# Kernel optimization log

Measured on AMD Instinct MI355X. Metric: run time of the kernel, lower is better.

## Reference

```python
import jax, jax.numpy as jnp
import numpy as np

B, S, D, H = 2, 2048, 1024, 16
HD = D // H
EPS = 1e-5

def _ln(x, g, b):
    mu = jnp.mean(x, axis=-1, keepdims=True)
    var = jnp.var(x, axis=-1, keepdims=True)
    return (x - mu) * jax.lax.rsqrt(var + EPS) * g + b

def setup_inputs() -> dict:
    key = jax.random.key(0)
    ks = jax.random.split(key, 6)
    sc = lambda n: 1.0 / np.sqrt(n)
    return {
        "x": jax.random.normal(ks[0], (B, S, D), jnp.float32),
        "W_qkv": jax.random.normal(ks[1], (D, 3 * D), jnp.float32) * sc(D),
        "b_qkv": jnp.zeros((3 * D,), jnp.float32),
        "W_o": jax.random.normal(ks[2], (D, D), jnp.float32) * sc(D),
        "b_o": jnp.zeros((D,), jnp.float32),
        "W_fc": jax.random.normal(ks[3], (D, 4 * D), jnp.float32) * sc(D),
        "b_fc": jnp.zeros((4 * D,), jnp.float32),
        "W_pr": jax.random.normal(ks[4], (4 * D, D), jnp.float32) * sc(4 * D),
        "b_pr": jnp.zeros((D,), jnp.float32),
        "g1": jnp.ones((D,), jnp.float32),
        "beta1": jnp.zeros((D,), jnp.float32),
        "g2": jnp.ones((D,), jnp.float32),
        "beta2": jnp.zeros((D,), jnp.float32),
    }

def reference(x, W_qkv, b_qkv, W_o, b_o, W_fc, b_fc, W_pr, b_pr, g1, beta1, g2, beta2):
    # pre-norm attention
    h = _ln(x, g1, beta1)
    qkv = h @ W_qkv + b_qkv                      # [B,S,3D]
    q, k, v = jnp.split(qkv, 3, axis=-1)
    q = q.reshape(B, S, H, HD).transpose(0, 2, 1, 3)  # [B,H,S,hd]
    k = k.reshape(B, S, H, HD).transpose(0, 2, 1, 3)
    v = v.reshape(B, S, H, HD).transpose(0, 2, 1, 3)
    scores = jnp.einsum('bhqd,bhkd->bhqk', q, k) / np.sqrt(HD)
    causal = jnp.tril(jnp.ones((S, S), bool))
    scores = jnp.where(causal, scores, -jnp.inf)
    attn = jax.nn.softmax(scores, axis=-1)
    out = jnp.einsum('bhqk,bhkd->bhqd', attn, v)
    out = out.transpose(0, 2, 1, 3).reshape(B, S, D)
    x = x + out @ W_o + b_o
    # pre-norm MLP (exact erf GELU, matching torch F.gelu default)
    h2 = _ln(x, g2, beta2)
    h2 = jax.nn.gelu(h2 @ W_fc + b_fc, approximate=False)
    x = x + h2 @ W_pr + b_pr
    return x
```

## Files before the change

### kernel.cpp

```cpp
#include <hip/hip_runtime.h>
#include <cstdint>
#include <cstddef>

#define Bb 2
#define Ss 2048
#define Dd 1024
#define Hh 16

typedef __attribute__((ext_vector_type(8))) short short8;
typedef __attribute__((ext_vector_type(4))) short short4v;
typedef __attribute__((ext_vector_type(4))) float float4v;

__device__ inline short f2bf(float f) {
  unsigned u = __builtin_bit_cast(unsigned, f);
  u = (u + 0x7fffu + ((u >> 16) & 1u)) >> 16;
  return (short)u;
}

__device__ inline float bf2f(short s) {
  unsigned u = ((unsigned)(unsigned short)s) << 16;
  return __builtin_bit_cast(float, u);
}

__device__ inline void gl_lds16(const void* g, void* l) {
  __builtin_amdgcn_global_load_lds(
      (__attribute__((address_space(1))) void*)(void*)(g),
      (__attribute__((address_space(3))) void*)(l), 16, 0, 0);
}

#define MFMA(a, b, c) __builtin_amdgcn_mfma_f32_16x16x32_bf16((a), (b), (c), 0, 0, 0)

__device__ __forceinline__ void ln_row(const float* __restrict__ x,
                                       const float* __restrict__ g,
                                       const float* __restrict__ be,
                                       short* __restrict__ out, int row,
                                       float* red) {
  int tid = threadIdx.x;
  const float4* xr = (const float4*)(x + (size_t)row * Dd);
  float4 v = xr[tid];
  float s = v.x + v.y + v.z + v.w;
  float q = v.x * v.x + v.y * v.y + v.z * v.z + v.w * v.w;
#pragma unroll
  for (int off = 1; off < 64; off <<= 1) {
    s += __shfl_xor(s, off);
    q += __shfl_xor(q, off);
  }
  int w = tid >> 6;
  if ((tid & 63) == 0) { red[w] = s; red[4 + w] = q; }
  __syncthreads();
  s = red[0] + red[1] + red[2] + red[3];
  q = red[4] + red[5] + red[6] + red[7];
  float mu = s * (1.0f / Dd);
  float var = q * (1.0f / Dd) - mu * mu;
  float rstd = rsqrtf(var + 1e-5f);
  float4 gv = ((const float4*)g)[tid], bv = ((const float4*)be)[tid];
  short4v o;
  o.x = f2bf((v.x - mu) * rstd * gv.x + bv.x);
  o.y = f2bf((v.y - mu) * rstd * gv.y + bv.y);
  o.z = f2bf((v.z - mu) * rstd * gv.z + bv.z);
  o.w = f2bf((v.w - mu) * rstd * gv.w + bv.w);
  *(short4v*)(out + (size_t)row * Dd + tid * 4) = o;
}

__global__ __launch_bounds__(256) void prep_kernel(
    const float* __restrict__ W0, short* __restrict__ T0,
    const float* __restrict__ W1, short* __restrict__ T1,
    const float* __restrict__ W2, short* __restrict__ T2,
    const float* __restrict__ W3, short* __restrict__ T3,
    const float* __restrict__ x, const float* __restrict__ g1,
    const float* __restrict__ be1, short* __restrict__ h1) {
  __shared__ __align__(16) float t[32][33];
  int id = blockIdx.x;
  if (id >= 12288) {
    ln_row(x, g1, be1, h1, id - 12288, &t[0][0]);
    return;
  }
  const float* W; short* Wt; int N, K, tix;
  if (id < 3072)      { W = W0; Wt = T0; N = 3072; K = 1024; tix = id; }
  else if (id < 4096) { W = W1; Wt = T1; N = 1024; K = 1024; tix = id - 3072; }
  else if (id < 8192) { W = W2; Wt = T2; N = 4096; K = 1024; tix = id - 4096; }
  else                { W = W3; Wt = T3; N = 1024; K = 4096; tix = id - 8192; }
  int nx = N / 32;
  int n0 = (tix % nx) * 32, k0 = (tix / nx) * 32;
  int tx = threadIdx.x & 31, ty = threadIdx.x >> 5;
#pragma unroll
  for (int i = 0; i < 4; i++)
    t[ty + 8 * i][tx] = W[(size_t)(k0 + ty + 8 * i) * N + n0 + tx];
  __syncthreads();
#pragma unroll
  for (int i = 0; i < 4; i++)
    Wt[(size_t)(n0 + ty + 8 * i) * K + k0 + tx] = f2bf(t[tx][ty + 8 * i]);
}

__global__ __launch_bounds__(256) void reduce_ln_kernel(const float* __restrict__ x,
                                                        const float* __restrict__ bias,
                                                        const short* __restrict__ parts,
                                                        const float* __restrict__ g,
                                                        const float* __restrict__ be,
                                                        float* __restrict__ x1,
                                                        short* __restrict__ h2) {
  int row = blockIdx.x, tid = threadIdx.x;
  size_t base = (size_t)row * Dd + tid * 4;
  float4 v = *(const float4*)(x + base);
  float4 bv = ((const float4*)bias)[tid];
  v.x += bv.x; v.y += bv.y; v.z += bv.z; v.w += bv.w;
#pragma unroll
  for (int s = 0; s < 2; s++) {
    short4v p = *(const short4v*)(parts + (size_t)s * 4096 * Dd + base);
    v.x += bf2f(p.x); v.y += bf2f(p.y); v.z += bf2f(p.z); v.w += bf2f(p.w);
  }
  *(float4*)(x1 + base) = v;
  float s = v.x + v.y + v.z + v.w;
  float q = v.x * v.x + v.y * v.y + v.z * v.z + v.w * v.w;
#pragma unroll
  for (int off = 1; off < 64; off <<= 1) {
    s += __shfl_xor(s, off);
    q += __shfl_xor(q, off);
  }
  __shared__ float as_[4], aq_[4];
  int w = tid >> 6;
  if ((tid & 63) == 0) { as_[w] = s; aq_[w] = q; }
  __syncthreads();
  s = as_[0] + as_[1] + as_[2] + as_[3];
  q = aq_[0] + aq_[1] + aq_[2] + aq_[3];
  float mu = s * (1.0f / Dd);
  float var = q * (1.0f / Dd) - mu * mu;
  float rstd = rsqrtf(var + 1e-5f);
  float4 gv = ((const float4*)g)[tid], b2 = ((const float4*)be)[tid];
  short4v o;
  o.x = f2bf((v.x - mu) * rstd * gv.x + b2.x);
  o.y = f2bf((v.y - mu) * rstd * gv.y + b2.y);
  o.z = f2bf((v.z - mu) * rstd * gv.z + b2.z);
  o.w = f2bf((v.w - mu) * rstd * gv.w + b2.w);
  *(short4v*)(h2 + base) = o;
}

__global__ __launch_bounds__(256) void reduce_kernel(const float* __restrict__ src,
                                                     const float* __restrict__ bias,
                                                     const short* __restrict__ parts,
                                                     float* __restrict__ dst) {
  int row = blockIdx.x, tid = threadIdx.x;
  size_t base = (size_t)row * Dd + tid * 4;
  float4 v = *(const float4*)(src + base);
  float4 bv = ((const float4*)bias)[tid];
  v.x += bv.x; v.y += bv.y; v.z += bv.z; v.w += bv.w;
#pragma unroll
  for (int s = 0; s < 2; s++) {
    short4v p = *(const short4v*)(parts + (size_t)s * 4096 * Dd + base);
    v.x += bf2f(p.x); v.y += bf2f(p.y); v.z += bf2f(p.z); v.w += bf2f(p.w);
  }
  *(float4*)(dst + base) = v;
}

template <int MODE>
__device__ __forceinline__ void gemm_tile(const short* __restrict__ A,
                                          const short* __restrict__ Bt,
                                          const float* __restrict__ bias,
                                          void* __restrict__ outp,
                                          short* __restrict__ vtp,
                                          int M, int N, int K,
                                          int m0, int n0, int zp,
                                          int ks, int ke, char* smem) {
  short* As = (short*)smem;
  short* Bs = (short*)smem + 128 * 64;
  const int tid = threadIdx.x;
  const int w = tid >> 6, lane = tid & 63;
  const int sr = lane >> 3;
  const int sc = lane & 7;
  const int gc = sc ^ sr;
  const int fr = lane & 15;
  const int g = lane >> 4;
  const int wm = (w >> 1) * 64, wn = (w & 1) * 64;
  float4v acc[4][4] = {};
  const short* Ag = A + (size_t)(m0 + w * 32 + sr) * K + gc * 8;
  const short* Bg = Bt + (size_t)(n0 + w * 32 + sr) * K + gc * 8;
  short* Asw = As + (w * 32 + sr) * 64 + sc * 8;
  short* Bsw = Bs + (w * 32 + sr) * 64 + sc * 8;
#pragma unroll
  for (int i = 0; i < 4; i++) {
    gl_lds16(Ag + (size_t)(i * 8) * K + ks, Asw + i * 8 * 64);
    gl_lds16(Bg + (size_t)(i * 8) * K + ks, Bsw + i * 8 * 64);
  }
  for (int k0 = ks; k0 < ke; k0 += 64) {
    __syncthreads();
    short8 a[2][4], b[2][4];
#pragma unroll
    for (int kh = 0; kh < 2; kh++) {
#pragma unroll
      for (int i = 0; i < 4; i++) {
        int row = wm + i * 16 + fr;
        int slot = (g + kh * 4) ^ (row & 7);
        a[kh][i] = *(const short8*)(As + row * 64 + slot * 8);
      }
#pragma unroll
      for (int j = 0; j < 4; j++) {
        int row = wn + j * 16 + fr;
        int slot = (g + kh * 4) ^ (row & 7);
        b[kh][j] = *(const short8*)(Bs + row * 64 + slot * 8);
      }
    }
    __syncthreads();
    if (k0 + 64 < ke) {
#pragma unroll
      for (int i = 0; i < 4; i++) {
        gl_lds16(Ag + (size_t)(i * 8) * K + k0 + 64, Asw + i * 8 * 64);
        gl_lds16(Bg + (size_t)(i * 8) * K + k0 + 64, Bsw + i * 8 * 64);
      }
    }
#pragma unroll
    for (int kh = 0; kh < 2; kh++)
#pragma unroll
      for (int i = 0; i < 4; i++)
#pragma unroll
        for (int j = 0; j < 4; j++)
          acc[kh & 0 ? 0 : i][j] = MFMA(a[kh][i], b[kh][j], acc[i][j]);
  }
  const int crow = g * 4;
  const int ccol = fr;
#pragma unroll
  for (int i = 0; i < 4; i++) {
#pragma unroll
    for (int j = 0; j < 4; j++) {
      int col = n0 + wn + j * 16 + ccol;
      float bcol = (MODE == 3) ? 0.f : bias[col];
      short sh[4];
#pragma unroll
      for (int r = 0; r < 4; r++) {
        int row = m0 + wm + i * 16 + crow + r;
        float v = acc[i][j][r] + bcol;
        if (MODE == 4) {
          sh[r] = f2bf(v);
          ((short*)outp)[(size_t)row * N + col] = sh[r];
        } else if (MODE == 2) {
          float y = 0.79788456f * (v + 0.044715f * v * v * v);
          float e = __builtin_amdgcn_exp2f(y * 2.885390082f);
          float th = 1.0f - 2.0f * __builtin_amdgcn_rcpf(e + 1.0f);
          v = 0.5f * v * (1.0f + th);
          ((short*)outp)[(size_t)row * N + col] = f2bf(v);
        } else {
          short* pp = (short*)outp + (size_t)zp * M * N;
          pp[(size_t)row * N + col] = f2bf(v);
        }
      }
      if (MODE == 4 && col >= 2048) {
        int hd = col - 2048;
        int rbase = m0 + wm + i * 16 + crow;
        int bq = rbase >> 11, sb = rbase & 2047;
        int bh = bq * 16 + (hd >> 6), d = hd & 63;
        short4v pk;
        pk.x = sh[0]; pk.y = sh[1]; pk.z = sh[2]; pk.w = sh[3];
        *(short4v*)(vtp + (size_t)(bh * 64 + d) * Ss + sb) = pk;
      }
    }
  }
}

__global__ __launch_bounds__(256) void k_gemm_qkv(const short* __restrict__ A,
                                                  const short* __restrict__ Bt,
                                                  const float* __restrict__ bias,
                                                  short* __restrict__ o,
                                                  short* __restrict__ Vt) {
  __shared__ __align__(16) char smem[32768];
  int t = blockIdx.x;
  int c8 = t & 7, tt = t >> 3;
  int m0 = ((c8 >> 1) * 8 + tt / 12) * 128;
  int n0 = ((c8 & 1) * 12 + tt % 12) * 128;
  gemm_tile<4>(A, Bt, bias, o, Vt, 4096, 3072, 1024, m0, n0, 0, 0, 1024, smem);
}

__global__ __launch_bounds__(256) void k_gemm_fc(const short* __restrict__ A,
                                                 const short* __restrict__ Bt,
                                                 const float* __restrict__ bias,
                                                 short* __restrict__ o) {
  __shared__ __align__(16) char smem[32768];
  int t = blockIdx.x;
  int c8 = t & 7, tt = t >> 3;
  int m0 = ((c8 >> 1) * 8 + tt / 16) * 128;
  int n0 = ((c8 & 1) * 16 + tt % 16) * 128;
  gemm_tile<2>(A, Bt, bias, o, nullptr, 4096, 4096, 1024, m0, n0, 0, 0, 1024, smem);
}

__global__ __launch_bounds__(256) void k_gemm_wo(const short* __restrict__ A,
                                                 const short* __restrict__ Bt,
                                                 short* __restrict__ parts) {
  __shared__ __align__(16) char smem[32768];
  int c = blockIdx.x;
  int z = c >> 8, rem = c & 255;
  int c8 = rem & 7, tt = rem >> 3;
  int m0 = (c8 * 4 + tt / 8) * 128, n0 = (tt % 8) * 128;
  gemm_tile<3>(A, Bt, nullptr, parts, nullptr, 4096, 1024, 1024, m0, n0, z,
               z * 512, z * 512 + 512, smem);
}

__global__ __launch_bounds__(256) void k_gemm_pr(const short* __restrict__ A,
                                                 const short* __restrict__ Bt,
                                                 short* __restrict__ parts) {
  __shared__ __align__(16) char smem[32768];
  int c = blockIdx.x;
  int z = c >> 8, rem = c & 255;
  int c8 = rem & 7, tt = rem >> 3;
  int m0 = (c8 * 4 + tt / 8) * 128, n0 = (tt % 8) * 128;
  gemm_tile<3>(A, Bt, nullptr, parts, nullptr, 4096, 1024, 4096, m0, n0, z,
               z * 2048, z * 2048 + 2048, smem);
}

__global__ __launch_bounds__(256) void flash_kernel(const short* __restrict__ qkv,
                                                    const short* __restrict__ Vt,
                                                    short* __restrict__ att) {
  __shared__ __align__(16) short Ks[4096];
  __shared__ __align__(16) short Vs[4096];
  __shared__ __align__(16) short P[4][16 * 72];
  const int w = threadIdx.x >> 6, lane = threadIdx.x & 63;
  const int qb = 31 - (blockIdx.x >> 5);
  const int bh = blockIdx.x & 31;
  const int b = bh >> 4, h = bh & 15;
  const int qbase = qb * 64 + w * 16;
  const int q = lane & 15;
  const int g = lane >> 4;
  const int fk = g * 8;
  short* Pw = &P[w][0];

  const int L0 = w * 64 + lane, L1 = L0 + 256;
  const int r0 = L0 >> 3, c0 = (L0 & 7) ^ (r0 & 7);
  const int r1 = L1 >> 3, c1 = (L1 & 7) ^ (r1 & 7);
  const short* kg0 = qkv + (size_t)(b * Ss + r0) * 3072 + 1024 + h * 64 + c0 * 8;
  const short* kg1 = qkv + (size_t)(b * Ss + r1) * 3072 + 1024 + h * 64 + c1 * 8;
  const short* vg0 = Vt + (size_t)(bh * 64 + r0) * Ss + c0 * 8;
  const short* vg1 = Vt + (size_t)(bh * 64 + r1) * Ss + c1 * 8;

  short8 qf[2];
  {
    const short* qrow = qkv + (size_t)(b * Ss + qbase + q) * 3072 + h * 64;
    qf[0] = *(const short8*)(qrow + fk);
    qf[1] = *(const short8*)(qrow + 32 + fk);
  }
  float4v o[4] = {};
  float l_i = 0.f;
  const float sc = 0.125f * 1.44269504088896f;
  const int nkt = qb + 1;

  gl_lds16(kg0, Ks + L0 * 8);
  gl_lds16(kg1, Ks + L1 * 8);
  gl_lds16(vg0, Vs + L0 * 8);
  gl_lds16(vg1, Vs + L1 * 8);

  for (int kt = 0; kt < nkt; kt++) {
    const int kbase = kt * 64;
    __syncthreads();

    short8 kf[4][2], vf[4][2];
#pragma unroll
    for (int t = 0; t < 4; t++) {
      const int row = 16 * t + q;
      const int sw = (g ^ (row & 7)) * 8;
      kf[t][0] = *(const short8*)(Ks + row * 64 + sw);
      kf[t][1] = *(const short8*)(Ks + row * 64 + (sw ^ 32));
      vf[t][0] = *(const short8*)(Vs + row * 64 + sw);
      vf[t][1] = *(const short8*)(Vs + row * 64 + (sw ^ 32));
    }
    __syncthreads();
    if (kt + 1 < nkt) {
      const size_t nb = (size_t)(kbase + 64);
      gl_lds16(kg0 + nb * 3072, Ks + L0 * 8);
      gl_lds16(kg1 + nb * 3072, Ks + L1 * 8);
      gl_lds16(vg0 + nb, Vs + L0 * 8);
      gl_lds16(vg1 + nb, Vs + L1 * 8);
    }

    float4v s[4] = {};
#pragma unroll
    for (int t = 0; t < 4; t++) {
      s[t] = MFMA(kf[t][0], qf[0], s[t]);
      s[t] = MFMA(kf[t][1], qf[1], s[t]);
    }
    const bool maskt = (kbase + 63 > qbase);
    const int qlim = qbase + q - kbase;
    float p[4][4];
    float rs = 0.f;
#pragma unroll
    for (int t = 0; t < 4; t++) {
#pragma unroll
      for (int r = 0; r < 4; r++) {
        float v = s[t][r] * sc;
        if (maskt && (16 * t + 4 * g + r > qlim)) v = -3.0e38f;
        float e = __builtin_amdgcn_exp2f(v);
        p[t][r] = e;
        rs += e;
      }
    }
    rs += __shfl_xor(rs, 16);
    rs += __shfl_xor(rs, 32);
    l_i += rs;
#pragma unroll
    for (int t = 0; t < 4; t++) {
      unsigned lo = (unsigned)(unsigned short)f2bf(p[t][0]) |
                    ((unsigned)(unsigned short)f2bf(p[t][1]) << 16);
      unsigned hi = (unsigned)(unsigned short)f2bf(p[t][2]) |
                    ((unsigned)(unsigned short)f2bf(p[t][3]) << 16);
      uint2 u; u.x = lo; u.y = hi;
      *(uint2*)(Pw + q * 72 + 16 * t + 4 * g) = u;
    }
    asm volatile("s_waitcnt lgkmcnt(0)" ::: "memory");
    short8 pb0 = *(const short8*)(Pw + q * 72 + fk);
    short8 pb1 = *(const short8*)(Pw + q * 72 + 32 + fk);
#pragma unroll
    for (int t = 0; t < 4; t++) {
      o[t] = MFMA(vf[t][0], pb0, o[t]);
      o[t] = MFMA(vf[t][1], pb1, o[t]);
    }
  }
  const float inv = 1.0f / l_i;
  const int orow = b * Ss + qbase + q;
#pragma unroll
  for (int t = 0; t < 4; t++) {
    short4v ov;
    ov.x = f2bf(o[t][0] * inv);
    ov.y = f2bf(o[t][1] * inv);
    ov.z = f2bf(o[t][2] * inv);
    ov.w = f2bf(o[t][3] * inv);
    *(short4v*)(att + (size_t)orow * Dd + h * 64 + 16 * t + 4 * g) = ov;
  }
}

extern "C" void kernel_launch(void* const* d_in, const int* in_sizes, int n_in,
                              void* d_out, int out_size, void* d_ws, size_t ws_size,
                              hipStream_t stream) {
  const float* x    = (const float*)d_in[0];
  const float* Wqkv = (const float*)d_in[1];
  const float* bqkv = (const float*)d_in[2];
  const float* Wo   = (const float*)d_in[3];
  const float* bo   = (const float*)d_in[4];
  const float* Wfc  = (const float*)d_in[5];
  const float* bfc  = (const float*)d_in[6];
  const float* Wpr  = (const float*)d_in[7];
  const float* bpr  = (const float*)d_in[8];
  const float* g1   = (const float*)d_in[9];
  const float* be1  = (const float*)d_in[10];
  const float* g2   = (const float*)d_in[11];
  const float* be2  = (const float*)d_in[12];

  char* ws = (char*)d_ws;
  const size_t MB = 1024 * 1024;
  short* h1     = (short*)(ws + 0);
  short* qkvb   = (short*)(ws + 8 * MB);
  short* partWo = (short*)(ws + 0);
  short* partPr = (short*)(ws + 0);
  short* Vt     = (short*)(ws + 32 * MB);
  short* att    = (short*)(ws + 40 * MB);
  float* x1     = (float*)(ws + 48 * MB);
  short* h2     = (short*)(ws + 64 * MB);
  short* geluo  = (short*)(ws + 72 * MB);
  short* WtQkv  = (short*)(ws + 104 * MB);
  short* WtO    = (short*)(ws + 110 * MB);
  short* WtFc   = (short*)(ws + 112 * MB);
  short* WtPr   = (short*)(ws + 120 * MB);

  prep_kernel<<<16384, 256, 0, stream>>>(Wqkv, WtQkv, Wo, WtO, Wfc, WtFc,
                                         Wpr, WtPr, x, g1, be1, h1);
  k_gemm_qkv<<<768, 256, 0, stream>>>(h1, WtQkv, bqkv, qkvb, Vt);
  flash_kernel<<<1024, 256, 0, stream>>>(qkvb, Vt, att);
  k_gemm_wo<<<512, 256, 0, stream>>>(att, WtO, partWo);
  reduce_ln_kernel<<<4096, 256, 0, stream>>>(x, bo, partWo, g2, be2, x1, h2);
  k_gemm_fc<<<1024, 256, 0, stream>>>(h2, WtFc, bfc, geluo);
  k_gemm_pr<<<512, 256, 0, stream>>>(geluo, WtPr, partPr);
  reduce_kernel<<<4096, 256, 0, stream>>>(x1, bpr, partPr, (float*)d_out);
}
```

Measured before the change: 294.9 us.

## Replace split-K partial buffers with intra-block split-K reduction and fused residual epilogue

The Wo and projection GEMMs now run 512-thread blocks where two 256-thread halves each compute half of K. The halves reduce through LDS, and the epilogue adds bias and residual, writing fp32 output directly. This removes the bf16 partial-sum buffers and the separate reduce kernel after the projection GEMM. The reduce+LN kernel is replaced by a plain LN kernel. The change also keeps the partial sums in fp32 instead of rounding them to bf16, and skips writing the V columns to the qkv buffer. Block count halves to 256, so a 256-CU device gets one block per CU, and each block needs 64KB of LDS.

New measurement: 309.2 us. +4.8%, slower.

```diff
diff --git a/kernel.cpp b/kernel.cpp
--- a/kernel.cpp
+++ b/kernel.cpp
@@ -92,64 +92,12 @@
     Wt[(size_t)(n0 + ty + 8 * i) * K + k0 + tx] = f2bf(t[tx][ty + 8 * i]);
 }
 
-__global__ __launch_bounds__(256) void reduce_ln_kernel(const float* __restrict__ x,
-                                                        const float* __restrict__ bias,
-                                                        const short* __restrict__ parts,
-                                                        const float* __restrict__ g,
-                                                        const float* __restrict__ be,
-                                                        float* __restrict__ x1,
-                                                        short* __restrict__ h2) {
-  int row = blockIdx.x, tid = threadIdx.x;
-  size_t base = (size_t)row * Dd + tid * 4;
-  float4 v = *(const float4*)(x + base);
-  float4 bv = ((const float4*)bias)[tid];
-  v.x += bv.x; v.y += bv.y; v.z += bv.z; v.w += bv.w;
-#pragma unroll
-  for (int s = 0; s < 2; s++) {
-    short4v p = *(const short4v*)(parts + (size_t)s * 4096 * Dd + base);
-    v.x += bf2f(p.x); v.y += bf2f(p.y); v.z += bf2f(p.z); v.w += bf2f(p.w);
-  }
-  *(float4*)(x1 + base) = v;
-  float s = v.x + v.y + v.z + v.w;
-  float q = v.x * v.x + v.y * v.y + v.z * v.z + v.w * v.w;
-#pragma unroll
-  for (int off = 1; off < 64; off <<= 1) {
-    s += __shfl_xor(s, off);
-    q += __shfl_xor(q, off);
-  }
-  __shared__ float as_[4], aq_[4];
-  int w = tid >> 6;
-  if ((tid & 63) == 0) { as_[w] = s; aq_[w] = q; }
-  __syncthreads();
-  s = as_[0] + as_[1] + as_[2] + as_[3];
-  q = aq_[0] + aq_[1] + aq_[2] + aq_[3];
-  float mu = s * (1.0f / Dd);
-  float var = q * (1.0f / Dd) - mu * mu;
-  float rstd = rsqrtf(var + 1e-5f);
-  float4 gv = ((const float4*)g)[tid], b2 = ((const float4*)be)[tid];
-  short4v o;
-  o.x = f2bf((v.x - mu) * rstd * gv.x + b2.x);
-  o.y = f2bf((v.y - mu) * rstd * gv.y + b2.y);
-  o.z = f2bf((v.z - mu) * rstd * gv.z + b2.z);
-  o.w = f2bf((v.w - mu) * rstd * gv.w + b2.w);
-  *(short4v*)(h2 + base) = o;
-}
-
-__global__ __launch_bounds__(256) void reduce_kernel(const float* __restrict__ src,
-                                                     const float* __restrict__ bias,
-                                                     const short* __restrict__ parts,
-                                                     float* __restrict__ dst) {
-  int row = blockIdx.x, tid = threadIdx.x;
-  size_t base = (size_t)row * Dd + tid * 4;
-  float4 v = *(const float4*)(src + base);
-  float4 bv = ((const float4*)bias)[tid];
-  v.x += bv.x; v.y += bv.y; v.z += bv.z; v.w += bv.w;
-#pragma unroll
-  for (int s = 0; s < 2; s++) {
-    short4v p = *(const short4v*)(parts + (size_t)s * 4096 * Dd + base);
-    v.x += bf2f(p.x); v.y += bf2f(p.y); v.z += bf2f(p.z); v.w += bf2f(p.w);
-  }
-  *(float4*)(dst + base) = v;
+__global__ __launch_bounds__(256) void ln2_kernel(const float* __restrict__ x1,
+                                                  const float* __restrict__ g,
+                                                  const float* __restrict__ be,
+                                                  short* __restrict__ h2) {
+  __shared__ float red[8];
+  ln_row(x1, g, be, h2, blockIdx.x, red);
 }
 
 template <int MODE>
@@ -159,7 +107,7 @@
                                           void* __restrict__ outp,
                                           short* __restrict__ vtp,
                                           int M, int N, int K,
-                                          int m0, int n0, int zp,
+                                          int m0, int n0,
                                           int ks, int ke, char* smem) {
   short* As = (short*)smem;
   short* Bs = (short*)smem + 128 * 64;
@@ -213,7 +161,7 @@
       for (int i = 0; i < 4; i++)
 #pragma unroll
         for (int j = 0; j < 4; j++)
-          acc[kh & 0 ? 0 : i][j] = MFMA(a[kh][i], b[kh][j], acc[i][j]);
+          acc[i][j] = MFMA(a[kh][i], b[kh][j], acc[i][j]);
   }
   const int crow = g * 4;
   const int ccol = fr;
@@ -222,7 +170,7 @@
 #pragma unroll
     for (int j = 0; j < 4; j++) {
       int col = n0 + wn + j * 16 + ccol;
-      float bcol = (MODE == 3) ? 0.f : bias[col];
+      float bcol = bias[col];
       short sh[4];
 #pragma unroll
       for (int r = 0; r < 4; r++) {
@@ -230,16 +178,13 @@
         float v = acc[i][j][r] + bcol;
         if (MODE == 4) {
           sh[r] = f2bf(v);
-          ((short*)outp)[(size_t)row * N + col] = sh[r];
-        } else if (MODE == 2) {
+          if (col < 2048) ((short*)outp)[(size_t)row * N + col] = sh[r];
+        } else {
           float y = 0.79788456f * (v + 0.044715f * v * v * v);
           float e = __builtin_amdgcn_exp2f(y * 2.885390082f);
           float th = 1.0f - 2.0f * __builtin_amdgcn_rcpf(e + 1.0f);
           v = 0.5f * v * (1.0f + th);
           ((short*)outp)[(size_t)row * N + col] = f2bf(v);
-        } else {
-          short* pp = (short*)outp + (size_t)zp * M * N;
-          pp[(size_t)row * N + col] = f2bf(v);
         }
       }
       if (MODE == 4 && col >= 2048) {
@@ -250,6 +195,98 @@
         short4v pk;
         pk.x = sh[0]; pk.y = sh[1]; pk.z = sh[2]; pk.w = sh[3];
         *(short4v*)(vtp + (size_t)(bh * 64 + d) * Ss + sb) = pk;
+      }
+    }
+  }
+}
+
+__device__ __forceinline__ void gemm_split_body(const short* __restrict__ A,
+                                                const short* __restrict__ Bt,
+                                                const float* __restrict__ bias,
+                                                const float* __restrict__ resid,
+                                                float* __restrict__ fout,
+                                                int M, int N, int K,
+                                                int m0, int n0, char* smem) {
+  const int half = threadIdx.x >> 8;
+  const int tid = threadIdx.x & 255;
+  const int w = tid >> 6, lane = tid & 63;
+  const int sr = lane >> 3, sc = lane & 7, gc = sc ^ sr;
+  const int fr = lane & 15, g = lane >> 4;
+  const int wm = (w >> 1) * 64, wn = (w & 1) * 64;
+  short* As = (short*)(smem + half * 32768);
+  short* Bs = (short*)(smem + half * 32768 + 16384);
+  const int ks = half * (K >> 1), ke = ks + (K >> 1);
+  float4v acc[4][4] = {};
+  const short* Ag = A + (size_t)(m0 + w * 32 + sr) * K + gc * 8;
+  const short* Bg = Bt + (size_t)(n0 + w * 32 + sr) * K + gc * 8;
+  short* Asw = As + (w * 32 + sr) * 64 + sc * 8;
+  short* Bsw = Bs + (w * 32 + sr) * 64 + sc * 8;
+#pragma unroll
+  for (int i = 0; i < 4; i++) {
+    gl_lds16(Ag + (size_t)(i * 8) * K + ks, Asw + i * 8 * 64);
+    gl_lds16(Bg + (size_t)(i * 8) * K + ks, Bsw + i * 8 * 64);
+  }
+  for (int k0 = ks; k0 < ke; k0 += 64) {
+    __syncthreads();
+    short8 a[2][4], b[2][4];
+#pragma unroll
+    for (int kh = 0; kh < 2; kh++) {
+#pragma unroll
+      for (int i = 0; i < 4; i++) {
+        int row = wm + i * 16 + fr;
+        int slot = (g + kh * 4) ^ (row & 7);
+        a[kh][i] = *(const short8*)(As + row * 64 + slot * 8);
+      }
+#pragma unroll
+      for (int j = 0; j < 4; j++) {
+        int row = wn + j * 16 + fr;
+        int slot = (g + kh * 4) ^ (row & 7);
+        b[kh][j] = *(const short8*)(Bs + row * 64 + slot * 8);
+      }
+    }
+    __syncthreads();
+    if (k0 + 64 < ke) {
+#pragma unroll
+      for (int i = 0; i < 4; i++) {
+        gl_lds16(Ag + (size_t)(i * 8) * K + k0 + 64, Asw + i * 8 * 64);
+        gl_lds16(Bg + (size_t)(i * 8) * K + k0 + 64, Bsw + i * 8 * 64);
+      }
+    }
+#pragma unroll
+    for (int kh = 0; kh < 2; kh++)
+#pragma unroll
+      for (int i = 0; i < 4; i++)
+#pragma unroll
+        for (int j = 0; j < 4; j++)
+          acc[i][j] = MFMA(a[kh][i], b[kh][j], acc[i][j]);
+  }
+  __syncthreads();
+  float* mb = (float*)smem;
+  if (half == 1) {
+#pragma unroll
+    for (int i = 0; i < 4; i++)
+#pragma unroll
+      for (int j = 0; j < 4; j++)
+#pragma unroll
+        for (int r = 0; r < 4; r++)
+          mb[(wm + i * 16 + g * 4 + r) * 128 + wn + j * 16 + fr] = acc[i][j][r];
+  }
+  __syncthreads();
+  if (half == 0) {
+#pragma unroll
+    for (int i = 0; i < 4; i++) {
+#pragma unroll
+      for (int j = 0; j < 4; j++) {
+        int col = n0 + wn + j * 16 + fr;
+        float bcol = bias[col];
+#pragma unroll
+        for (int r = 0; r < 4; r++) {
+          int row = m0 + wm + i * 16 + g * 4 + r;
+          float v = acc[i][j][r] +
+                    mb[(wm + i * 16 + g * 4 + r) * 128 + wn + j * 16 + fr] +
+                    bcol + resid[(size_t)row * N + col];
+          fout[(size_t)row * N + col] = v;
+        }
       }
     }
   }
@@ -265,7 +302,7 @@
   int c8 = t & 7, tt = t >> 3;
   int m0 = ((c8 >> 1) * 8 + tt / 12) * 128;
   int n0 = ((c8 & 1) * 12 + tt % 12) * 128;
-  gemm_tile<4>(A, Bt, bias, o, Vt, 4096, 3072, 1024, m0, n0, 0, 0, 1024, smem);
+  gemm_tile<4>(A, Bt, bias, o, Vt, 4096, 3072, 1024, m0, n0, 0, 1024, smem);
 }
 
 __global__ __launch_bounds__(256) void k_gemm_fc(const short* __restrict__ A,
@@ -277,31 +314,31 @@
   int c8 = t & 7, tt = t >> 3;
   int m0 = ((c8 >> 1) * 8 + tt / 16) * 128;
   int n0 = ((c8 & 1) * 16 + tt % 16) * 128;
-  gemm_tile<2>(A, Bt, bias, o, nullptr, 4096, 4096, 1024, m0, n0, 0, 0, 1024, smem);
-}
-
-__global__ __launch_bounds__(256) void k_gemm_wo(const short* __restrict__ A,
+  gemm_tile<2>(A, Bt, bias, o, nullptr, 4096, 4096, 1024, m0, n0, 0, 1024, smem);
+}
+
+__global__ __launch_bounds__(512) void k_gemm_wo(const short* __restrict__ A,
                                                  const short* __restrict__ Bt,
-                                                 short* __restrict__ parts) {
-  __shared__ __align__(16) char smem[32768];
+                                                 const float* __restrict__ bias,
+                                                 const float* __restrict__ resid,
+                                                 float* __restrict__ fout) {
+  __shared__ __align__(16) char smem[65536];
   int c = blockIdx.x;
-  int z = c >> 8, rem = c & 255;
-  int c8 = rem & 7, tt = rem >> 3;
+  int c8 = c & 7, tt = c >> 3;
   int m0 = (c8 * 4 + tt / 8) * 128, n0 = (tt % 8) * 128;
-  gemm_tile<3>(A, Bt, nullptr, parts, nullptr, 4096, 1024, 1024, m0, n0, z,
-               z * 512, z * 512 + 512, smem);
-}
-
-__global__ __launch_bounds__(256) void k_gemm_pr(const short* __restrict__ A,
+  gemm_split_body(A, Bt, bias, resid, fout, 4096, 1024, 1024, m0, n0, smem);
+}
+
+__global__ __launch_bounds__(512) void k_gemm_pr(const short* __restrict__ A,
                                                  const short* __restrict__ Bt,
-                                                 short* __restrict__ parts) {
-  __shared__ __align__(16) char smem[32768];
+                                                 const float* __restrict__ bias,
+                                                 const float* __restrict__ resid,
+                                                 float* __restrict__ fout) {
+  __shared__ __align__(16) char smem[65536];
   int c = blockIdx.x;
-  int z = c >> 8, rem = c & 255;
-  int c8 = rem & 7, tt = rem >> 3;
+  int c8 = c & 7, tt = c >> 3;
   int m0 = (c8 * 4 + tt / 8) * 128, n0 = (tt % 8) * 128;
-  gemm_tile<3>(A, Bt, nullptr, parts, nullptr, 4096, 1024, 4096, m0, n0, z,
-               z * 2048, z * 2048 + 2048, smem);
+  gemm_split_body(A, Bt, bias, resid, fout, 4096, 1024, 4096, m0, n0, smem);
 }
 
 __global__ __launch_bounds__(256) void flash_kernel(const short* __restrict__ qkv,
@@ -443,8 +480,6 @@
   const size_t MB = 1024 * 1024;
   short* h1     = (short*)(ws + 0);
   short* qkvb   = (short*)(ws + 8 * MB);
-  short* partWo = (short*)(ws + 0);
-  short* partPr = (short*)(ws + 0);
   short* Vt     = (short*)(ws + 32 * MB);
   short* att    = (short*)(ws + 40 * MB);
   float* x1     = (float*)(ws + 48 * MB);
@@ -459,9 +494,8 @@
                                          Wpr, WtPr, x, g1, be1, h1);
   k_gemm_qkv<<<768, 256, 0, stream>>>(h1, WtQkv, bqkv, qkvb, Vt);
   flash_kernel<<<1024, 256, 0, stream>>>(qkvb, Vt, att);
-  k_gemm_wo<<<512, 256, 0, stream>>>(att, WtO, partWo);
-  reduce_ln_kernel<<<4096, 256, 0, stream>>>(x, bo, partWo, g2, be2, x1, h2);
+  k_gemm_wo<<<256, 512, 0, stream>>>(att, WtO, bo, x, x1);
+  ln2_kernel<<<4096, 256, 0, stream>>>(x1, g2, be2, h2);
   k_gemm_fc<<<1024, 256, 0, stream>>>(h2, WtFc, bfc, geluo);
-  k_gemm_pr<<<512, 256, 0, stream>>>(geluo, WtPr, partPr);
-  reduce_kernel<<<4096, 256, 0, stream>>>(x1, bpr, partPr, (float*)d_out);
-}
+  k_gemm_pr<<<256, 512, 0, stream>>>(geluo, WtPr, bpr, x1, (float*)d_out);
+}
```
